# Optimization experiments

Measured on AMD Instinct MI355X. Metric: run time of the kernel, lower is better.

## Reference

```python
import jax, jax.numpy as jnp
import numpy as np

H, C, L = 4, 64, 3          # heads, out_channels, conv layers
N, E, B = 20000, 320000, 32 # nodes, edges, graphs
HD = 64                     # hidden_dim


def setup_inputs() -> dict:
    key = jax.random.key(0)
    ks = jax.random.split(key, 24)
    x = jax.random.normal(ks[0], (N, 3), jnp.float32)
    src = jax.random.randint(ks[1], (E,), 0, N)
    dst = jax.random.randint(ks[2], (E,), 0, N)
    dst = jnp.where(dst == src, (dst + 1) % N, dst)  # no pre-existing self loops
    edge_index = jnp.stack([src, dst])
    edge_attr = jax.random.normal(ks[3], (E, 4), jnp.float32)
    u = jax.random.normal(ks[4], (B, 10), jnp.float32)
    batch = jnp.sort(jax.random.randint(ks[5], (N,), 0, B))
    p = lambda k, s: jax.random.normal(k, s, jnp.float32) * 0.1
    return {
        'x': x, 'edge_index': edge_index, 'edge_attr': edge_attr, 'u': u, 'batch': batch,
        'node_W': p(ks[6], (3, HD)), 'node_b': p(ks[7], (HD,)),
        'eemb_W': p(ks[8], (4, HD)), 'eemb_b': p(ks[9], (HD,)),
        'lin_W': p(ks[10], (L, HD, H * C)),
        'att_src': p(ks[11], (L, H, C)), 'att_dst': p(ks[12], (L, H, C)),
        'lin_eW': p(ks[13], (L, HD, H * C)), 'att_e': p(ks[14], (L, H, C)),
        'conv_b': p(ks[15], (L, C)),
        'gW': p(ks[16], (10, HD)), 'gb': p(ks[17], (HD,)),
        'f1W': p(ks[18], (2 * HD, HD)), 'f1b': p(ks[19], (HD,)),
        'f2W': p(ks[20], (HD, 2)), 'f2b': p(ks[21], (2,)),
    }


def _gat_layer(x, src, dst, ea, W, a_src, a_dst, We, a_e, b):
    # PyG GATConv(hidden, hidden, edge_dim=hidden, heads=4, concat=False), eval mode
    n = x.shape[0]
    # add self loops; self-loop edge_attr = mean of incoming edge_attr (fill_value='mean')
    deg = jax.ops.segment_sum(jnp.ones_like(dst, dtype=x.dtype), dst, num_segments=n)
    ea_self = jax.ops.segment_sum(ea, dst, num_segments=n) / jnp.maximum(deg, 1.0)[:, None]
    loop = jnp.arange(n)
    src2 = jnp.concatenate([src, loop])
    dst2 = jnp.concatenate([dst, loop])
    ea2 = jnp.concatenate([ea, ea_self], axis=0)
    xp = (x @ W).reshape(n, H, C)                       # [N,H,C]
    a_s = jnp.einsum('nhc,hc->nh', xp, a_src)           # [N,H]
    a_d = jnp.einsum('nhc,hc->nh', xp, a_dst)
    ee = (ea2 @ We).reshape(-1, H, C)                   # [E2,H,C]
    a_ed = jnp.einsum('ehc,hc->eh', ee, a_e)
    alpha = jax.nn.leaky_relu(a_s[src2] + a_d[dst2] + a_ed, 0.2)  # [E2,H]
    # segment softmax over destination nodes (stable)
    m = jax.ops.segment_max(alpha, dst2, num_segments=n)
    ex = jnp.exp(alpha - m[dst2])
    den = jax.ops.segment_sum(ex, dst2, num_segments=n)
    att = ex / den[dst2]
    out = jax.ops.segment_sum(xp[src2] * att[..., None], dst2, num_segments=n)  # [N,H,C]
    return out.mean(axis=1) + b  # concat=False -> mean over heads


def reference(x, edge_index, edge_attr, u, batch, node_W, node_b, eemb_W, eemb_b,
              lin_W, att_src, att_dst, lin_eW, att_e, conv_b, gW, gb, f1W, f1b, f2W, f2b):
    src, dst = edge_index[0], edge_index[1]
    h = jax.nn.relu(x @ node_W + node_b)
    ea = jax.nn.relu(edge_attr @ eemb_W + eemb_b)
    for i in range(L):
        h = jax.nn.relu(_gat_layer(h, src, dst, ea, lin_W[i], att_src[i], att_dst[i],
                                   lin_eW[i], att_e[i], conv_b[i]))
    # global mean pool over graphs
    cnt = jax.ops.segment_sum(jnp.ones((h.shape[0],), h.dtype), batch, num_segments=B)
    pooled = jax.ops.segment_sum(h, batch, num_segments=B) / jnp.maximum(cnt, 1.0)[:, None]
    ug = jax.nn.relu(u @ gW + gb)
    z = jnp.concatenate([pooled, ug], axis=1)
    z = jax.nn.relu(z @ f1W + f1b)
    return z @ f2W + f2b
```

## Files before the change

kernel.cpp:

```cpp
#include <hip/hip_runtime.h>
#include <hip/hip_bf16.h>

#define HD 64

typedef unsigned short u16;

__device__ __forceinline__ float lrelu(float x) { return x > 0.f ? x : 0.2f * x; }
__device__ __forceinline__ int clampi(int v, int maxv) {
    return v < 0 ? 0 : (v >= maxv ? maxv - 1 : v);
}
__device__ __forceinline__ float bf2f(u16 u) {
    return __uint_as_float(((unsigned int)u) << 16);
}
__device__ __forceinline__ float bflo(unsigned int u) { return __uint_as_float(u << 16); }
__device__ __forceinline__ float bfhi(unsigned int u) { return __uint_as_float(u & 0xffff0000u); }
__device__ __forceinline__ u16 f2bf(float f) {
    unsigned int u = __float_as_uint(f);
    unsigned int lsb = (u >> 16) & 1u;
    u += 0x7fffu + lsb;
    return (u16)(u >> 16);
}

__global__ void k_init(const float* __restrict__ x, const float* __restrict__ W,
                       const float* __restrict__ b, float* __restrict__ h,
                       const float* __restrict__ lin_W, const float* __restrict__ att_src,
                       const float* __restrict__ att_dst, float* __restrict__ wsd,
                       int* deg, int* cursor, float* pooled, int N, int B) {
    int i = blockIdx.x * blockDim.x + threadIdx.x;
    if (i < N) { deg[i] = 0; cursor[i] = 0; }
    if (i < B * HD) pooled[i] = 0.f;
    if (i < 3 * 512) {
        int l = i >> 9, r = i & 511;
        int idx = r >> 6, d = r & 63;
        int hh = idx >> 1, sel = idx & 1;
        const float* att = (sel ? att_dst : att_src) + l * 256 + hh * 64;
        const float* Wrow = lin_W + (size_t)l * HD * 256 + d * 256 + hh * 64;
        float acc = 0.f;
        for (int c = 0; c < 64; c++) acc = fmaf(Wrow[c], att[c], acc);
        wsd[(l << 9) + (idx << 6) + d] = acc;
    }
    if (i < N * HD) {
        int n = i >> 6, c = i & 63;
        float acc = b[c];
        acc = fmaf(x[n * 3 + 0], W[0 * HD + c], acc);
        acc = fmaf(x[n * 3 + 1], W[1 * HD + c], acc);
        acc = fmaf(x[n * 3 + 2], W[2 * HD + c], acc);
        h[i] = fmaxf(acc, 0.f);
    }
}

__global__ void k_deg(const int* __restrict__ dst, int* __restrict__ deg, int E, int N) {
    int e = blockIdx.x * blockDim.x + threadIdx.x;
    if (e < E) atomicAdd(&deg[clampi(dst[e], N)], 1);
}

__global__ void k_scan1(const int* __restrict__ deg, int* __restrict__ tmp,
                        int* __restrict__ bsum, int N) {
    __shared__ int s[256];
    int tid = threadIdx.x;
    int i = blockIdx.x * 256 + tid;
    int v = (i < N) ? deg[i] : 0;
    s[tid] = v;
    __syncthreads();
    for (int off = 1; off < 256; off <<= 1) {
        int t = (tid >= off) ? s[tid - off] : 0;
        __syncthreads();
        s[tid] += t;
        __syncthreads();
    }
    if (i < N) tmp[i] = s[tid];
    if (tid == 255) bsum[blockIdx.x] = s[255];
}
__global__ void k_scan23(const int* __restrict__ tmp, const int* __restrict__ bsum,
                         int* __restrict__ row_ptr, int N) {
    __shared__ int s_off;
    int t = threadIdx.x;
    if (t < 64) {
        int cnt = blockIdx.x;
        int v = 0;
        for (int base = 0; base < cnt; base += 64)
            if (base + t < cnt) v += bsum[base + t];
        #pragma unroll
        for (int o = 32; o > 0; o >>= 1) v += __shfl_xor(v, o);
        if (t == 0) s_off = v;
    }
    __syncthreads();
    int i = blockIdx.x * 256 + t;
    if (i == 0) row_ptr[0] = 0;
    if (i < N) row_ptr[i + 1] = tmp[i] + s_off;
}

__global__ void k_csr(const int* __restrict__ src, const int* __restrict__ dst,
                      const int* __restrict__ row_ptr, int* __restrict__ cursor,
                      int2* __restrict__ csr_se, int E, int N) {
    int e = blockIdx.x * blockDim.x + threadIdx.x;
    if (e >= E) return;
    int d = clampi(dst[e], N);
    int pos = row_ptr[d] + atomicAdd(&cursor[d], 1);
    if (pos < E) csr_se[pos] = make_int2(clampi(src[e], N), e);
}

__global__ __launch_bounds__(256) void k_ee(
    const float* __restrict__ edge_attr, const float* __restrict__ eW,
    const float* __restrict__ eB, const float* __restrict__ lin_eW,
    const float* __restrict__ att_e, const int2* __restrict__ csr_se,
    float* __restrict__ aed, int E, int N) {
    __shared__ float s_ew[256];
    __shared__ float s_eb[64];
    __shared__ float s_wred[768];
    size_t P4 = (size_t)(E + N) * 4;
    int t = threadIdx.x;
    s_ew[t] = eW[t];
    if (t < 64) s_eb[t] = eB[t];
    for (int idx = t; idx < 768; idx += 256) {
        int l = idx >> 8, hd = idx & 255, hh = hd >> 6, d = hd & 63;
        const float* We = lin_eW + (size_t)l * HD * 256;
        const float* ae = att_e + (size_t)l * 256;
        float acc = 0.f;
        for (int c = 0; c < 64; c++)
            acc = fmaf(We[d * 256 + hh * 64 + c], ae[hh * 64 + c], acc);
        s_wred[idx] = acc;
    }
    __syncthreads();
    int j0 = (blockIdx.x * 256 + t) * 4;
    if (j0 >= E) return;
    float4 a[4];
    int nv = 0;
    #pragma unroll
    for (int q = 0; q < 4; q++) {
        int j = j0 + q;
        if (j < E) {
            a[q] = *(const float4*)(edge_attr + (size_t)csr_se[j].y * 4);
            nv = q + 1;
        } else {
            a[q] = make_float4(0.f, 0.f, 0.f, 0.f);
        }
    }
    float acc[4][12];
    #pragma unroll
    for (int q = 0; q < 4; q++)
        #pragma unroll
        for (int m = 0; m < 12; m++) acc[q][m] = 0.f;
    for (int k = 0; k < HD; k++) {
        float e0 = s_ew[k], e1 = s_ew[64 + k], e2 = s_ew[128 + k], e3 = s_ew[192 + k];
        float eb = s_eb[k];
        float w[12];
        #pragma unroll
        for (int m = 0; m < 12; m++)
            w[m] = s_wred[(m >> 2) * 256 + (m & 3) * 64 + k];
        #pragma unroll
        for (int q = 0; q < 4; q++) {
            float v = fmaf(a[q].x, e0, fmaf(a[q].y, e1,
                      fmaf(a[q].z, e2, fmaf(a[q].w, e3, eb))));
            v = fmaxf(v, 0.f);
            #pragma unroll
            for (int m = 0; m < 12; m++) acc[q][m] = fmaf(v, w[m], acc[q][m]);
        }
    }
    #pragma unroll
    for (int q = 0; q < 4; q++) {
        if (q >= nv) break;
        #pragma unroll
        for (int l = 0; l < 3; l++) {
            *(float4*)(aed + l * P4 + (size_t)(j0 + q) * 4) =
                make_float4(acc[q][l * 4 + 0], acc[q][l * 4 + 1],
                            acc[q][l * 4 + 2], acc[q][l * 4 + 3]);
        }
    }
}

__global__ void k_selfed(const int* __restrict__ row_ptr, float* __restrict__ aed,
                         int E, int N) {
    int n = blockIdx.x * blockDim.x + threadIdx.x;
    if (n >= N) return;
    size_t P4 = (size_t)(E + N) * 4;
    int r0 = row_ptr[n], r1 = row_ptr[n + 1];
    float acc[12];
    #pragma unroll
    for (int m = 0; m < 12; m++) acc[m] = 0.f;
    for (int j = r0; j < r1; j++) {
        #pragma unroll
        for (int l = 0; l < 3; l++) {
            float4 v = *(const float4*)(aed + l * P4 + (size_t)j * 4);
            acc[l * 4 + 0] += v.x; acc[l * 4 + 1] += v.y;
            acc[l * 4 + 2] += v.z; acc[l * 4 + 3] += v.w;
        }
    }
    float inv = 1.f / fmaxf((float)(r1 - r0), 1.f);
    #pragma unroll
    for (int l = 0; l < 3; l++) {
        *(float4*)(aed + l * P4 + (size_t)(E + n) * 4) =
            make_float4(acc[l * 4 + 0] * inv, acc[l * 4 + 1] * inv,
                        acc[l * 4 + 2] * inv, acc[l * 4 + 3] * inv);
    }
}

#define NPB 8
__global__ __launch_bounds__(256) void k_xp(
    const float* __restrict__ h, const float* __restrict__ W,
    const float* __restrict__ wsdl, u16* __restrict__ xp,
    float* __restrict__ a_s, float* __restrict__ a_d, int N) {
    int n0 = blockIdx.x * NPB;
    int c = threadIdx.x;
    int nlim = N - n0;
    const float* hp = h + (size_t)n0 * HD;
    float acc[NPB];
    #pragma unroll
    for (int k = 0; k < NPB; k++) acc[k] = 0.f;
    for (int d = 0; d < HD; d += 4) {
        float w0 = W[(d + 0) * 256 + c];
        float w1 = W[(d + 1) * 256 + c];
        float w2 = W[(d + 2) * 256 + c];
        float w3 = W[(d + 3) * 256 + c];
        #pragma unroll
        for (int k = 0; k < NPB; k++) {
            int kk = (k < nlim) ? k : 0;
            float4 hv = *(const float4*)(hp + kk * HD + d);
            acc[k] = fmaf(hv.x, w0, acc[k]);
            acc[k] = fmaf(hv.y, w1, acc[k]);
            acc[k] = fmaf(hv.z, w2, acc[k]);
            acc[k] = fmaf(hv.w, w3, acc[k]);
        }
    }
    int hh = c >> 6, cc = c & 63;
    #pragma unroll
    for (int k = 0; k < NPB; k++) {
        int nn = n0 + k;
        if (nn >= N) break;
        xp[(size_t)nn * 256 + cc * 4 + hh] = f2bf(acc[k]);
    }
    if (c < 64) {
        int k = c >> 3, idx = c & 7;
        int nn = n0 + k;
        if (nn < N) {
            const float* hr = hp + k * HD;
            const float* wp = wsdl + (idx << 6);
            float a = 0.f;
            for (int d = 0; d < HD; d += 4) {
                float4 hv = *(const float4*)(hr + d);
                float4 wv = *(const float4*)(wp + d);
                a = fmaf(hv.x, wv.x, a);
                a = fmaf(hv.y, wv.y, a);
                a = fmaf(hv.z, wv.z, a);
                a = fmaf(hv.w, wv.w, a);
            }
            int hd = idx >> 1, sel = idx & 1;
            if (sel) a_d[nn * 4 + hd] = a;
            else     a_s[nn * 4 + hd] = a;
        }
    }
}

__global__ __launch_bounds__(256) void k_gat(
    const u16* __restrict__ xp, const float* __restrict__ a_s,
    const float* __restrict__ a_d, const float* __restrict__ aedl,
    const int* __restrict__ row_ptr, const int2* __restrict__ csr_se,
    const float* __restrict__ convb, float* __restrict__ h_out, int N, int E) {
    int wave = threadIdx.x >> 6, lane = threadIdx.x & 63;
    int n = blockIdx.x * 4 + wave;
    if (n >= N) return;
    int g = lane >> 4, p = lane & 15;
    int r0 = row_ptr[n], r1 = row_ptr[n + 1];
    float4 ad4 = *(const float4*)(a_d + (size_t)n * 4);
    float a00 = 0.f, a01 = 0.f, a02 = 0.f, a03 = 0.f;
    float a10 = 0.f, a11 = 0.f, a12 = 0.f, a13 = 0.f;
    float a20 = 0.f, a21 = 0.f, a22 = 0.f, a23 = 0.f;
    float a30 = 0.f, a31 = 0.f, a32 = 0.f, a33 = 0.f;
    float d0 = 0.f, d1 = 0.f, d2 = 0.f, d3 = 0.f;
    if (g == 0) {
        float4 as4 = *(const float4*)(a_s + (size_t)n * 4);
        float4 p4 = *(const float4*)(aedl + (size_t)(E + n) * 4);
        float w0 = __expf(lrelu(as4.x + ad4.x + p4.x));
        float w1 = __expf(lrelu(as4.y + ad4.y + p4.y));
        float w2 = __expf(lrelu(as4.z + ad4.z + p4.z));
        float w3 = __expf(lrelu(as4.w + ad4.w + p4.w));
        const u16* row = xp + (size_t)n * 256 + p * 16;
        uint4 q0 = *(const uint4*)(row);
        uint4 q1 = *(const uint4*)(row + 8);
        d0 += w0; d1 += w1; d2 += w2; d3 += w3;
        a00 = fmaf(w0, bflo(q0.x), a00); a01 = fmaf(w0, bflo(q0.z), a01);
        a02 = fmaf(w0, bflo(q1.x), a02); a03 = fmaf(w0, bflo(q1.z), a03);
        a10 = fmaf(w1, bfhi(q0.x), a10); a11 = fmaf(w1, bfhi(q0.z), a11);
        a12 = fmaf(w1, bfhi(q1.x), a12); a13 = fmaf(w1, bfhi(q1.z), a13);
        a20 = fmaf(w2, bflo(q0.y), a20); a21 = fmaf(w2, bflo(q0.w), a21);
        a22 = fmaf(w2, bflo(q1.y), a22); a23 = fmaf(w2, bflo(q1.w), a23);
        a30 = fmaf(w3, bfhi(q0.y), a30); a31 = fmaf(w3, bfhi(q0.w), a31);
        a32 = fmaf(w3, bfhi(q1.y), a32); a33 = fmaf(w3, bfhi(q1.w), a33);
    }
    int j = r0 + g;
    int2 se = (j < r1) ? csr_se[j] : make_int2(0, 0);
    for (; j < r1; j += 4) {
        int jn = j + 4;
        int2 se_n = (jn < r1) ? csr_se[jn] : make_int2(0, 0);
        int s = se.x;
        float4 as4 = *(const float4*)(a_s + (size_t)s * 4);
        float4 p4 = *(const float4*)(aedl + (size_t)j * 4);
        float w0 = __expf(lrelu(as4.x + ad4.x + p4.x));
        float w1 = __expf(lrelu(as4.y + ad4.y + p4.y));
        float w2 = __expf(lrelu(as4.z + ad4.z + p4.z));
        float w3 = __expf(lrelu(as4.w + ad4.w + p4.w));
        const u16* row = xp + (size_t)s * 256 + p * 16;
        uint4 q0 = *(const uint4*)(row);
        uint4 q1 = *(const uint4*)(row + 8);
        d0 += w0; d1 += w1; d2 += w2; d3 += w3;
        a00 = fmaf(w0, bflo(q0.x), a00); a01 = fmaf(w0, bflo(q0.z), a01);
        a02 = fmaf(w0, bflo(q1.x), a02); a03 = fmaf(w0, bflo(q1.z), a03);
        a10 = fmaf(w1, bfhi(q0.x), a10); a11 = fmaf(w1, bfhi(q0.z), a11);
        a12 = fmaf(w1, bfhi(q1.x), a12); a13 = fmaf(w1, bfhi(q1.z), a13);
        a20 = fmaf(w2, bflo(q0.y), a20); a21 = fmaf(w2, bflo(q0.w), a21);
        a22 = fmaf(w2, bflo(q1.y), a22); a23 = fmaf(w2, bflo(q1.w), a23);
        a30 = fmaf(w3, bfhi(q0.y), a30); a31 = fmaf(w3, bfhi(q0.w), a31);
        a32 = fmaf(w3, bfhi(q1.y), a32); a33 = fmaf(w3, bfhi(q1.w), a33);
        se = se_n;
    }
    d0 += __shfl_xor(d0, 16); d0 += __shfl_xor(d0, 32);
    d1 += __shfl_xor(d1, 16); d1 += __shfl_xor(d1, 32);
    d2 += __shfl_xor(d2, 16); d2 += __shfl_xor(d2, 32);
    d3 += __shfl_xor(d3, 16); d3 += __shfl_xor(d3, 32);
    float i0 = 1.f / d0, i1 = 1.f / d1, i2 = 1.f / d2, i3 = 1.f / d3;
    float m0 = a00 * i0 + a10 * i1 + a20 * i2 + a30 * i3;
    float m1 = a01 * i0 + a11 * i1 + a21 * i2 + a31 * i3;
    float m2 = a02 * i0 + a12 * i1 + a22 * i2 + a32 * i3;
    float m3 = a03 * i0 + a13 * i1 + a23 * i2 + a33 * i3;
    m0 += __shfl_xor(m0, 16); m0 += __shfl_xor(m0, 32);
    m1 += __shfl_xor(m1, 16); m1 += __shfl_xor(m1, 32);
    m2 += __shfl_xor(m2, 16); m2 += __shfl_xor(m2, 32);
    m3 += __shfl_xor(m3, 16); m3 += __shfl_xor(m3, 32);
    if (lane < 16) {
        int c = p * 4;
        h_out[(size_t)n * HD + c + 0] = fmaxf(0.25f * m0 + convb[c + 0], 0.f);
        h_out[(size_t)n * HD + c + 1] = fmaxf(0.25f * m1 + convb[c + 1], 0.f);
        h_out[(size_t)n * HD + c + 2] = fmaxf(0.25f * m2 + convb[c + 2], 0.f);
        h_out[(size_t)n * HD + c + 3] = fmaxf(0.25f * m3 + convb[c + 3], 0.f);
    }
}

#define PCHUNK 8
__global__ void k_pool(const float* __restrict__ h, const int* __restrict__ batch,
                       float* __restrict__ pooled, int N, int B) {
    int b = blockIdx.x / PCHUNK, q = blockIdx.x % PCHUNK;
    __shared__ int sb[2];
    __shared__ float sred[256];
    int t = threadIdx.x;
    if (t == 0 || t == 64) {
        int target = b + (t ? 1 : 0);
        int lo = 0, hi = N;
        while (lo < hi) {
            int m = (lo + hi) >> 1;
            if (batch[m] < target) lo = m + 1; else hi = m;
        }
        sb[t ? 1 : 0] = lo;
    }
    __syncthreads();
    int start = sb[0], end = sb[1];
    int len = end - start;
    int c0 = start + (int)(((long long)len * q) / PCHUNK);
    int c1 = start + (int)(((long long)len * (q + 1)) / PCHUNK);
    int c = t & 63, r = t >> 6;
    float acc = 0.f;
    for (int nidx = c0 + r; nidx < c1; nidx += 4)
        acc += h[(size_t)nidx * HD + c];
    sred[t] = acc;
    __syncthreads();
    if (t < 64) {
        float v = sred[t] + sred[64 + t] + sred[128 + t] + sred[192 + t];
        if (v != 0.f) atomicAdd(&pooled[b * HD + c], v);
    }
}

__global__ void k_mlp(const float* __restrict__ u, const float* __restrict__ gW,
                      const float* __restrict__ gb, const float* __restrict__ pooled,
                      const int* __restrict__ batch, const float* __restrict__ f1W,
                      const float* __restrict__ f1b, const float* __restrict__ f2W,
                      const float* __restrict__ f2b, float* __restrict__ out,
                      int N, int B) {
    __shared__ float z[2 * HD];
    __shared__ float z1s[HD];
    __shared__ int sb[2];
    int b = blockIdx.x, t = threadIdx.x;
    if (t < 2) {
        int target = b + t;
        int lo = 0, hi = N;
        while (lo < hi) {
            int m = (lo + hi) >> 1;
            if (batch[m] < target) lo = m + 1; else hi = m;
        }
        sb[t] = lo;
    }
    float acc = gb[t];
    for (int k = 0; k < 10; k++) acc = fmaf(u[b * 10 + k], gW[k * HD + t], acc);
    z[HD + t] = fmaxf(acc, 0.f);
    __syncthreads();
    float invc = 1.f / fmaxf((float)(sb[1] - sb[0]), 1.f);
    z[t] = pooled[b * HD + t] * invc;
    __syncthreads();
    float a1 = f1b[t];
    for (int k = 0; k < 2 * HD; k++) a1 = fmaf(z[k], f1W[k * HD + t], a1);
    z1s[t] = fmaxf(a1, 0.f);
    __syncthreads();
    if (t < 2) {
        float o = f2b[t];
        for (int k = 0; k < HD; k++) o = fmaf(z1s[k], f2W[k * 2 + t], o);
        out[b * 2 + t] = o;
    }
}

extern "C" void kernel_launch(void* const* d_in, const int* in_sizes, int n_in,
                              void* d_out, int out_size, void* d_ws, size_t ws_size,
                              hipStream_t stream) {
    const float* x         = (const float*)d_in[0];
    const int*   ei        = (const int*)d_in[1];
    const float* edge_attr = (const float*)d_in[2];
    const float* u         = (const float*)d_in[3];
    const int*   batch     = (const int*)d_in[4];
    const float* node_W    = (const float*)d_in[5];
    const float* node_b    = (const float*)d_in[6];
    const float* eemb_W    = (const float*)d_in[7];
    const float* eemb_b    = (const float*)d_in[8];
    const float* lin_W     = (const float*)d_in[9];
    const float* att_src   = (const float*)d_in[10];
    const float* att_dst   = (const float*)d_in[11];
    const float* lin_eW    = (const float*)d_in[12];
    const float* att_e     = (const float*)d_in[13];
    const float* conv_b    = (const float*)d_in[14];
    const float* gW        = (const float*)d_in[15];
    const float* gb        = (const float*)d_in[16];
    const float* f1W       = (const float*)d_in[17];
    const float* f1b       = (const float*)d_in[18];
    const float* f2W       = (const float*)d_in[19];
    const float* f2b       = (const float*)d_in[20];

    const int N = in_sizes[0] / 3;
    const int E = in_sizes[2] / 4;
    const int B = in_sizes[3] / 10;
    const int* src = ei;
    const int* dst = ei + E;
    const int NB = (N + 255) / 256;
    const size_t P4 = (size_t)(E + N) * 4;

    float* wsf = (float*)d_ws;
    float* h       = wsf;              wsf += (size_t)N * HD;
    float* a_s     = wsf;              wsf += (size_t)N * 4;
    float* a_d     = wsf;              wsf += (size_t)N * 4;
    float* aed     = wsf;              wsf += 3 * P4;
    float* pooled  = wsf;              wsf += (size_t)B * HD;
    float* wsd     = wsf;              wsf += 3 * 512;
    u16* xp = (u16*)wsf;               wsf += (size_t)N * 128;
    int* wsi = (int*)wsf;
    int2* csr_se = (int2*)wsi;         wsi += 2 * (size_t)E;
    int* deg     = wsi;                wsi += N;
    int* row_ptr = wsi;                wsi += N + 1;
    int* cursor  = wsi;                wsi += N;
    int* tmp     = wsi;                wsi += N;
    int* bsum    = wsi;                wsi += NB + 1;

    k_init<<<(N * HD + 255) / 256, 256, 0, stream>>>(x, node_W, node_b, h,
                                                     lin_W, att_src, att_dst, wsd,
                                                     deg, cursor, pooled, N, B);
    k_deg<<<(E + 255) / 256, 256, 0, stream>>>(dst, deg, E, N);
    k_scan1<<<NB, 256, 0, stream>>>(deg, tmp, bsum, N);
    k_scan23<<<NB, 256, 0, stream>>>(tmp, bsum, row_ptr, N);
    k_csr<<<(E + 255) / 256, 256, 0, stream>>>(src, dst, row_ptr, cursor,
                                               csr_se, E, N);
    k_ee<<<(E + 1023) / 1024, 256, 0, stream>>>(edge_attr, eemb_W, eemb_b, lin_eW, att_e,
                                                csr_se, aed, E, N);
    k_selfed<<<NB, 256, 0, stream>>>(row_ptr, aed, E, N);
    for (int i = 0; i < 3; i++) {
        k_xp<<<(N + NPB - 1) / NPB, 256, 0, stream>>>(h, lin_W + (size_t)i * HD * 256,
                                                      wsd + (size_t)i * 512,
                                                      xp, a_s, a_d, N);
        k_gat<<<(N + 3) / 4, 256, 0, stream>>>(xp, a_s, a_d, aed + (size_t)i * P4,
                                               row_ptr, csr_se,
                                               conv_b + (size_t)i * HD, h, N, E);
    }
    k_pool<<<B * PCHUNK, 256, 0, stream>>>(h, batch, pooled, N, B);
    k_mlp<<<B, 64, 0, stream>>>(u, gW, gb, pooled, batch, f1W, f1b, f2W, f2b,
                                (float*)d_out, N, B);
}
```

Before: 369.1 us.

## Aggregate raw features before projection, applying lin_W after the GAT gather

Attention aggregation is moved ahead of the linear projection: k_gat now gathers 64-wide fp32 h rows per head instead of 256-wide bf16 projected rows, and a new k_post kernel multiplies the aggregated per-head features by lin_W. k_post also applies bias and relu and computes the next layer's attention logits, while a separate k_att computes the first layer's logits. This cuts gather width per edge but makes the per-node matmul four times larger (256 inputs) and adds an intermediate bf16 buffer round trip. Accumulators across heads are now all reduced via shuffles, which adds shuffle work.

```diff
diff --git a/kernel.cpp b/kernel.cpp
--- a/kernel.cpp
+++ b/kernel.cpp
@@ -12,8 +12,6 @@
 __device__ __forceinline__ float bf2f(u16 u) {
     return __uint_as_float(((unsigned int)u) << 16);
 }
-__device__ __forceinline__ float bflo(unsigned int u) { return __uint_as_float(u << 16); }
-__device__ __forceinline__ float bfhi(unsigned int u) { return __uint_as_float(u & 0xffff0000u); }
 __device__ __forceinline__ u16 f2bf(float f) {
     unsigned int u = __float_as_uint(f);
     unsigned int lsb = (u >> 16) & 1u;
@@ -47,6 +45,25 @@
         acc = fmaf(x[n * 3 + 2], W[2 * HD + c], acc);
         h[i] = fmaxf(acc, 0.f);
     }
+}
+
+__global__ void k_att(const float* __restrict__ h, const float* __restrict__ wsdl,
+                      float* __restrict__ a_s, float* __restrict__ a_d, int N) {
+    int i = blockIdx.x * blockDim.x + threadIdx.x;
+    if (i >= N * 8) return;
+    int n = i >> 3, idx = i & 7;
+    const float* hr = h + (size_t)n * HD;
+    const float* wp = wsdl + (idx << 6);
+    float a = 0.f;
+    for (int d = 0; d < HD; d += 4) {
+        float4 hv = *(const float4*)(hr + d);
+        float4 wv = *(const float4*)(wp + d);
+        a = fmaf(hv.x, wv.x, a); a = fmaf(hv.y, wv.y, a);
+        a = fmaf(hv.z, wv.z, a); a = fmaf(hv.w, wv.w, a);
+    }
+    int hd = idx >> 1, sel = idx & 1;
+    if (sel) a_d[n * 4 + hd] = a;
+    else     a_s[n * 4 + hd] = a;
 }
 
 __global__ void k_deg(const int* __restrict__ dst, int* __restrict__ deg, int E, int N) {
@@ -195,67 +212,11 @@
     }
 }
 
-#define NPB 8
-__global__ __launch_bounds__(256) void k_xp(
-    const float* __restrict__ h, const float* __restrict__ W,
-    const float* __restrict__ wsdl, u16* __restrict__ xp,
-    float* __restrict__ a_s, float* __restrict__ a_d, int N) {
-    int n0 = blockIdx.x * NPB;
-    int c = threadIdx.x;
-    int nlim = N - n0;
-    const float* hp = h + (size_t)n0 * HD;
-    float acc[NPB];
-    #pragma unroll
-    for (int k = 0; k < NPB; k++) acc[k] = 0.f;
-    for (int d = 0; d < HD; d += 4) {
-        float w0 = W[(d + 0) * 256 + c];
-        float w1 = W[(d + 1) * 256 + c];
-        float w2 = W[(d + 2) * 256 + c];
-        float w3 = W[(d + 3) * 256 + c];
-        #pragma unroll
-        for (int k = 0; k < NPB; k++) {
-            int kk = (k < nlim) ? k : 0;
-            float4 hv = *(const float4*)(hp + kk * HD + d);
-            acc[k] = fmaf(hv.x, w0, acc[k]);
-            acc[k] = fmaf(hv.y, w1, acc[k]);
-            acc[k] = fmaf(hv.z, w2, acc[k]);
-            acc[k] = fmaf(hv.w, w3, acc[k]);
-        }
-    }
-    int hh = c >> 6, cc = c & 63;
-    #pragma unroll
-    for (int k = 0; k < NPB; k++) {
-        int nn = n0 + k;
-        if (nn >= N) break;
-        xp[(size_t)nn * 256 + cc * 4 + hh] = f2bf(acc[k]);
-    }
-    if (c < 64) {
-        int k = c >> 3, idx = c & 7;
-        int nn = n0 + k;
-        if (nn < N) {
-            const float* hr = hp + k * HD;
-            const float* wp = wsdl + (idx << 6);
-            float a = 0.f;
-            for (int d = 0; d < HD; d += 4) {
-                float4 hv = *(const float4*)(hr + d);
-                float4 wv = *(const float4*)(wp + d);
-                a = fmaf(hv.x, wv.x, a);
-                a = fmaf(hv.y, wv.y, a);
-                a = fmaf(hv.z, wv.z, a);
-                a = fmaf(hv.w, wv.w, a);
-            }
-            int hd = idx >> 1, sel = idx & 1;
-            if (sel) a_d[nn * 4 + hd] = a;
-            else     a_s[nn * 4 + hd] = a;
-        }
-    }
-}
-
 __global__ __launch_bounds__(256) void k_gat(
-    const u16* __restrict__ xp, const float* __restrict__ a_s,
+    const float* __restrict__ h, const float* __restrict__ a_s,
     const float* __restrict__ a_d, const float* __restrict__ aedl,
     const int* __restrict__ row_ptr, const int2* __restrict__ csr_se,
-    const float* __restrict__ convb, float* __restrict__ h_out, int N, int E) {
+    u16* __restrict__ z, int N, int E) {
     int wave = threadIdx.x >> 6, lane = threadIdx.x & 63;
     int n = blockIdx.x * 4 + wave;
     if (n >= N) return;
@@ -274,18 +235,16 @@
         float w1 = __expf(lrelu(as4.y + ad4.y + p4.y));
         float w2 = __expf(lrelu(as4.z + ad4.z + p4.z));
         float w3 = __expf(lrelu(as4.w + ad4.w + p4.w));
-        const u16* row = xp + (size_t)n * 256 + p * 16;
-        uint4 q0 = *(const uint4*)(row);
-        uint4 q1 = *(const uint4*)(row + 8);
+        float4 hv = *(const float4*)(h + (size_t)n * HD + p * 4);
         d0 += w0; d1 += w1; d2 += w2; d3 += w3;
-        a00 = fmaf(w0, bflo(q0.x), a00); a01 = fmaf(w0, bflo(q0.z), a01);
-        a02 = fmaf(w0, bflo(q1.x), a02); a03 = fmaf(w0, bflo(q1.z), a03);
-        a10 = fmaf(w1, bfhi(q0.x), a10); a11 = fmaf(w1, bfhi(q0.z), a11);
-        a12 = fmaf(w1, bfhi(q1.x), a12); a13 = fmaf(w1, bfhi(q1.z), a13);
-        a20 = fmaf(w2, bflo(q0.y), a20); a21 = fmaf(w2, bflo(q0.w), a21);
-        a22 = fmaf(w2, bflo(q1.y), a22); a23 = fmaf(w2, bflo(q1.w), a23);
-        a30 = fmaf(w3, bfhi(q0.y), a30); a31 = fmaf(w3, bfhi(q0.w), a31);
-        a32 = fmaf(w3, bfhi(q1.y), a32); a33 = fmaf(w3, bfhi(q1.w), a33);
+        a00 = fmaf(w0, hv.x, a00); a01 = fmaf(w0, hv.y, a01);
+        a02 = fmaf(w0, hv.z, a02); a03 = fmaf(w0, hv.w, a03);
+        a10 = fmaf(w1, hv.x, a10); a11 = fmaf(w1, hv.y, a11);
+        a12 = fmaf(w1, hv.z, a12); a13 = fmaf(w1, hv.w, a13);
+        a20 = fmaf(w2, hv.x, a20); a21 = fmaf(w2, hv.y, a21);
+        a22 = fmaf(w2, hv.z, a22); a23 = fmaf(w2, hv.w, a23);
+        a30 = fmaf(w3, hv.x, a30); a31 = fmaf(w3, hv.y, a31);
+        a32 = fmaf(w3, hv.z, a32); a33 = fmaf(w3, hv.w, a33);
     }
     int j = r0 + g;
     int2 se = (j < r1) ? csr_se[j] : make_int2(0, 0);
@@ -299,39 +258,108 @@
         float w1 = __expf(lrelu(as4.y + ad4.y + p4.y));
         float w2 = __expf(lrelu(as4.z + ad4.z + p4.z));
         float w3 = __expf(lrelu(as4.w + ad4.w + p4.w));
-        const u16* row = xp + (size_t)s * 256 + p * 16;
-        uint4 q0 = *(const uint4*)(row);
-        uint4 q1 = *(const uint4*)(row + 8);
+        float4 hv = *(const float4*)(h + (size_t)s * HD + p * 4);
         d0 += w0; d1 += w1; d2 += w2; d3 += w3;
-        a00 = fmaf(w0, bflo(q0.x), a00); a01 = fmaf(w0, bflo(q0.z), a01);
-        a02 = fmaf(w0, bflo(q1.x), a02); a03 = fmaf(w0, bflo(q1.z), a03);
-        a10 = fmaf(w1, bfhi(q0.x), a10); a11 = fmaf(w1, bfhi(q0.z), a11);
-        a12 = fmaf(w1, bfhi(q1.x), a12); a13 = fmaf(w1, bfhi(q1.z), a13);
-        a20 = fmaf(w2, bflo(q0.y), a20); a21 = fmaf(w2, bflo(q0.w), a21);
-        a22 = fmaf(w2, bflo(q1.y), a22); a23 = fmaf(w2, bflo(q1.w), a23);
-        a30 = fmaf(w3, bfhi(q0.y), a30); a31 = fmaf(w3, bfhi(q0.w), a31);
-        a32 = fmaf(w3, bfhi(q1.y), a32); a33 = fmaf(w3, bfhi(q1.w), a33);
+        a00 = fmaf(w0, hv.x, a00); a01 = fmaf(w0, hv.y, a01);
+        a02 = fmaf(w0, hv.z, a02); a03 = fmaf(w0, hv.w, a03);
+        a10 = fmaf(w1, hv.x, a10); a11 = fmaf(w1, hv.y, a11);
+        a12 = fmaf(w1, hv.z, a12); a13 = fmaf(w1, hv.w, a13);
+        a20 = fmaf(w2, hv.x, a20); a21 = fmaf(w2, hv.y, a21);
+        a22 = fmaf(w2, hv.z, a22); a23 = fmaf(w2, hv.w, a23);
+        a30 = fmaf(w3, hv.x, a30); a31 = fmaf(w3, hv.y, a31);
+        a32 = fmaf(w3, hv.z, a32); a33 = fmaf(w3, hv.w, a33);
         se = se_n;
     }
     d0 += __shfl_xor(d0, 16); d0 += __shfl_xor(d0, 32);
     d1 += __shfl_xor(d1, 16); d1 += __shfl_xor(d1, 32);
     d2 += __shfl_xor(d2, 16); d2 += __shfl_xor(d2, 32);
     d3 += __shfl_xor(d3, 16); d3 += __shfl_xor(d3, 32);
-    float i0 = 1.f / d0, i1 = 1.f / d1, i2 = 1.f / d2, i3 = 1.f / d3;
-    float m0 = a00 * i0 + a10 * i1 + a20 * i2 + a30 * i3;
-    float m1 = a01 * i0 + a11 * i1 + a21 * i2 + a31 * i3;
-    float m2 = a02 * i0 + a12 * i1 + a22 * i2 + a32 * i3;
-    float m3 = a03 * i0 + a13 * i1 + a23 * i2 + a33 * i3;
-    m0 += __shfl_xor(m0, 16); m0 += __shfl_xor(m0, 32);
-    m1 += __shfl_xor(m1, 16); m1 += __shfl_xor(m1, 32);
-    m2 += __shfl_xor(m2, 16); m2 += __shfl_xor(m2, 32);
-    m3 += __shfl_xor(m3, 16); m3 += __shfl_xor(m3, 32);
+    a00 += __shfl_xor(a00, 16); a00 += __shfl_xor(a00, 32);
+    a01 += __shfl_xor(a01, 16); a01 += __shfl_xor(a01, 32);
+    a02 += __shfl_xor(a02, 16); a02 += __shfl_xor(a02, 32);
+    a03 += __shfl_xor(a03, 16); a03 += __shfl_xor(a03, 32);
+    a10 += __shfl_xor(a10, 16); a10 += __shfl_xor(a10, 32);
+    a11 += __shfl_xor(a11, 16); a11 += __shfl_xor(a11, 32);
+    a12 += __shfl_xor(a12, 16); a12 += __shfl_xor(a12, 32);
+    a13 += __shfl_xor(a13, 16); a13 += __shfl_xor(a13, 32);
+    a20 += __shfl_xor(a20, 16); a20 += __shfl_xor(a20, 32);
+    a21 += __shfl_xor(a21, 16); a21 += __shfl_xor(a21, 32);
+    a22 += __shfl_xor(a22, 16); a22 += __shfl_xor(a22, 32);
+    a23 += __shfl_xor(a23, 16); a23 += __shfl_xor(a23, 32);
+    a30 += __shfl_xor(a30, 16); a30 += __shfl_xor(a30, 32);
+    a31 += __shfl_xor(a31, 16); a31 += __shfl_xor(a31, 32);
+    a32 += __shfl_xor(a32, 16); a32 += __shfl_xor(a32, 32);
+    a33 += __shfl_xor(a33, 16); a33 += __shfl_xor(a33, 32);
     if (lane < 16) {
-        int c = p * 4;
-        h_out[(size_t)n * HD + c + 0] = fmaxf(0.25f * m0 + convb[c + 0], 0.f);
-        h_out[(size_t)n * HD + c + 1] = fmaxf(0.25f * m1 + convb[c + 1], 0.f);
-        h_out[(size_t)n * HD + c + 2] = fmaxf(0.25f * m2 + convb[c + 2], 0.f);
-        h_out[(size_t)n * HD + c + 3] = fmaxf(0.25f * m3 + convb[c + 3], 0.f);
+        float i0 = 1.f / d0, i1 = 1.f / d1, i2 = 1.f / d2, i3 = 1.f / d3;
+        u16* zr = z + (size_t)n * 256 + p * 4;
+        *(ushort4*)(zr)       = make_ushort4(f2bf(a00 * i0), f2bf(a01 * i0),
+                                             f2bf(a02 * i0), f2bf(a03 * i0));
+        *(ushort4*)(zr + 64)  = make_ushort4(f2bf(a10 * i1), f2bf(a11 * i1),
+                                             f2bf(a12 * i1), f2bf(a13 * i1));
+        *(ushort4*)(zr + 128) = make_ushort4(f2bf(a20 * i2), f2bf(a21 * i2),
+                                             f2bf(a22 * i2), f2bf(a23 * i2));
+        *(ushort4*)(zr + 192) = make_ushort4(f2bf(a30 * i3), f2bf(a31 * i3),
+                                             f2bf(a32 * i3), f2bf(a33 * i3));
+    }
+}
+
+#define PNB 8
+__global__ __launch_bounds__(256) void k_post(
+    const u16* __restrict__ z, const float* __restrict__ W,
+    const float* __restrict__ convb, const float* __restrict__ wsdn,
+    float* __restrict__ h_out, float* __restrict__ a_s, float* __restrict__ a_d, int N) {
+    __shared__ float sred[4 * PNB * 64];
+    __shared__ float hnew[PNB * 64];
+    int t = threadIdx.x;
+    int c = t & 63, kq = t >> 6;
+    int n0 = blockIdx.x * PNB;
+    int nlim = N - n0;
+    const u16* zp = z + (size_t)n0 * 256;
+    float acc[PNB];
+    #pragma unroll
+    for (int m = 0; m < PNB; m++) acc[m] = 0.f;
+    for (int kk = 0; kk < 16; kk++) {
+        int k4 = kq * 64 + kk * 4;
+        int base = (k4 >> 6) * 64 + c;
+        float wv0 = W[((k4 & 63) + 0) * 256 + base];
+        float wv1 = W[((k4 & 63) + 1) * 256 + base];
+        float wv2 = W[((k4 & 63) + 2) * 256 + base];
+        float wv3 = W[((k4 & 63) + 3) * 256 + base];
+        #pragma unroll
+        for (int m = 0; m < PNB; m++) {
+            int mm = (m < nlim) ? m : 0;
+            ushort4 zz = *(const ushort4*)(zp + (size_t)mm * 256 + k4);
+            acc[m] = fmaf(bf2f(zz.x), wv0, acc[m]);
+            acc[m] = fmaf(bf2f(zz.y), wv1, acc[m]);
+            acc[m] = fmaf(bf2f(zz.z), wv2, acc[m]);
+            acc[m] = fmaf(bf2f(zz.w), wv3, acc[m]);
+        }
+    }
+    #pragma unroll
+    for (int m = 0; m < PNB; m++) sred[(kq * PNB + m) * 64 + c] = acc[m];
+    __syncthreads();
+    if (kq == 0) {
+        #pragma unroll
+        for (int m = 0; m < PNB; m++) {
+            float v = sred[m * 64 + c] + sred[(PNB + m) * 64 + c] +
+                      sred[(2 * PNB + m) * 64 + c] + sred[(3 * PNB + m) * 64 + c];
+            v = fmaxf(0.25f * v + convb[c], 0.f);
+            hnew[m * 64 + c] = v;
+            if (m < nlim) h_out[(size_t)(n0 + m) * HD + c] = v;
+        }
+    }
+    __syncthreads();
+    if (t < PNB * 8) {
+        int m = t >> 3, idx = t & 7;
+        if (m < nlim) {
+            const float* wp = wsdn + (idx << 6);
+            float a = 0.f;
+            for (int d = 0; d < HD; d++) a = fmaf(hnew[m * 64 + d], wp[d], a);
+            int hd = idx >> 1, sel = idx & 1;
+            if (sel) a_d[(size_t)(n0 + m) * 4 + hd] = a;
+            else     a_s[(size_t)(n0 + m) * 4 + hd] = a;
+        }
     }
 }
 
@@ -445,7 +473,7 @@
     float* aed     = wsf;              wsf += 3 * P4;
     float* pooled  = wsf;              wsf += (size_t)B * HD;
     float* wsd     = wsf;              wsf += 3 * 512;
-    u16* xp = (u16*)wsf;               wsf += (size_t)N * 128;
+    u16* zbuf = (u16*)wsf;             wsf += (size_t)N * 128;
     int* wsi = (int*)wsf;
     int2* csr_se = (int2*)wsi;         wsi += 2 * (size_t)E;
     int* deg     = wsi;                wsi += N;
@@ -465,13 +493,15 @@
     k_ee<<<(E + 1023) / 1024, 256, 0, stream>>>(edge_attr, eemb_W, eemb_b, lin_eW, att_e,
                                                 csr_se, aed, E, N);
     k_selfed<<<NB, 256, 0, stream>>>(row_ptr, aed, E, N);
+    k_att<<<(N * 8 + 255) / 256, 256, 0, stream>>>(h, wsd, a_s, a_d, N);
     for (int i = 0; i < 3; i++) {
-        k_xp<<<(N + NPB - 1) / NPB, 256, 0, stream>>>(h, lin_W + (size_t)i * HD * 256,
-                                                      wsd + (size_t)i * 512,
-                                                      xp, a_s, a_d, N);
-        k_gat<<<(N + 3) / 4, 256, 0, stream>>>(xp, a_s, a_d, aed + (size_t)i * P4,
-                                               row_ptr, csr_se,
-                                               conv_b + (size_t)i * HD, h, N, E);
+        k_gat<<<(N + 3) / 4, 256, 0, stream>>>(h, a_s, a_d, aed + (size_t)i * P4,
+                                               row_ptr, csr_se, zbuf, N, E);
+        const float* wsdn = wsd + (size_t)(i < 2 ? i + 1 : 2) * 512;
+        k_post<<<(N + PNB - 1) / PNB, 256, 0, stream>>>(zbuf,
+                                                        lin_W + (size_t)i * HD * 256,
+                                                        conv_b + (size_t)i * HD,
+                                                        wsdn, h, a_s, a_d, N);
     }
     k_pool<<<B * PCHUNK, 256, 0, stream>>>(h, batch, pooled, N, B);
     k_mlp<<<B, 64, 0, stream>>>(u, gW, gb, pooled, batch, f1W, f1b, f2W, f2b,
```

After: 447.0 us. +21.1%, slower.
